# Kernel optimization log

Measured on AMD Instinct MI355X. Metric: run time of the kernel, lower is better.

## Reference

```python
import jax, jax.numpy as jnp
from jax import lax
import numpy as np

BS = 16          # batch (must be even, K % BS == 0)
K = 8192         # MoCo queue size
H = 768          # hidden size
G = 5            # rank_num (number of GMM components)
UPDATE_MEAN = 0.1


def _norm(x):
    return x / jnp.linalg.norm(x, axis=-1, keepdims=True)


def setup_inputs() -> dict:
    key = jax.random.key(0)
    ks = jax.random.split(key, 6)
    sent_q = _norm(jax.random.normal(ks[0], (BS, H), jnp.float32))
    sent_k = _norm(jax.random.normal(ks[1], (BS, H), jnp.float32))
    queue = _norm(jax.random.normal(ks[2], (K, H), jnp.float32))
    mu = jax.random.normal(ks[3], (G, H), jnp.float32)
    lg_sigma2 = jax.random.normal(ks[4], (G, H), jnp.float32)
    pi = jnp.ones((G,), jnp.float32)
    rank_mean = jax.random.uniform(ks[5], (G,), jnp.float32)
    return {"sent_q": sent_q, "sent_k": sent_k, "queue": queue,
            "mu": mu, "lg_sigma2": lg_sigma2, "pi": pi, "rank_mean": rank_mean}


def gaussian_mixture(features, mu, lg_sigma2, pi):
    # features: [B, N, H]; mu/lg_sigma2: [G, H]; pi: [G]
    # expo_{bng} = sum_h (f_{bnh} - mu_{gh})^2 / sigma2_{gh}, expanded so we never
    # materialize the [B, N, G, H] diff tensor the torch code builds.
    inv = jnp.exp(-lg_sigma2)                                   # [G, H]
    expo = (jnp.einsum('bnh,gh->bng', features * features, inv)
            - 2.0 * jnp.einsum('bnh,gh->bng', features, mu * inv)
            + jnp.sum(mu * mu * inv, axis=-1))                  # [B, N, G]
    lg2piD = features.shape[-1] * np.log(2.0 * np.pi).astype(np.float32)
    l_prob = -0.5 * (lg2piD + jnp.sum(lg_sigma2, axis=-1) + expo)
    logits = jax.nn.log_softmax(pi) + l_prob
    logits_norm = logits - jnp.max(logits, axis=-1, keepdims=True)
    prob = jax.nn.softmax(logits_norm, axis=-1)
    return logits_norm, prob


def reference(sent_q, sent_k, queue, mu, lg_sigma2, pi, rank_mean):
    bs = sent_q.shape[0]
    all_feature = jnp.concatenate([sent_k, queue], axis=0)       # [N, H]
    N = all_feature.shape[0]

    # golden mask (is_pair=True): pair j of i is (i + bs//2) mod bs
    pair_label = jnp.concatenate([jnp.arange(bs)[bs // 2:], jnp.arange(bs)[:bs // 2]])
    golden = jnp.arange(bs)[:, None] == pair_label[None, :]      # [bs, bs]
    golden_mask = jnp.concatenate(
        [golden, jnp.zeros((bs, N - bs), bool)], axis=1)         # [bs, N]

    sample_sim = sent_q @ all_feature.T                          # [bs, N]

    # map_scores_to_ranks (rank_mean detached)
    rm = lax.stop_gradient(rank_mean)
    cts_pred = jnp.argmin(jnp.abs(sample_sim[..., None] - rm[None, None, :]), axis=-1)
    cts_dist = jnp.floor((sample_sim + 1.0) / 2.0 * G).astype(jnp.int32)

    # GMM on detached broadcast diff [bs, N, H]
    f = lax.stop_gradient(sent_q)[:, None, :] - lax.stop_gradient(all_feature)[None, :, :]
    gmm_logits, gmm_prob = gaussian_mixture(f, mu, lg_sigma2, pi)
    gmm_pred = jnp.argmax(gmm_prob, axis=-1)                     # [bs, N]

    eye = jnp.arange(bs)[:, None] == jnp.arange(N)[None, :]      # [bs, N]
    # torch: gmm_label aliases cts_pred and is masked_fill_'d in place
    gmm_label = jnp.where(eye | golden_mask, G - 1, cts_pred)

    # update_rank_mean(sample_sim, gmm_pred) -- uses gmm_pred BEFORE cts_label masking
    oh = jax.nn.one_hot(gmm_pred, G, dtype=sample_sim.dtype)     # [bs, N, G]
    counts = jnp.sum(oh, axis=(0, 1))                            # [G]
    sums = jnp.einsum('bng,bn->g', oh, sample_sim)
    cur_rank_mean = sums / (counts + 1e-12)
    upd = (counts != 0).astype(rank_mean.dtype)
    new_rank_mean = (1.0 - upd * UPDATE_MEAN) * rank_mean + upd * UPDATE_MEAN * cur_rank_mean

    # torch: cts_label aliases gmm_pred and masked_fill_ mutates both in place;
    # the returned 'gmm pred' therefore equals this masked version.
    cts_label = jnp.where(golden_mask, G - 1, gmm_pred)

    logits_max = lax.stop_gradient(jnp.max(sample_sim, axis=1, keepdims=True))
    cts_logits = sample_sim - logits_max

    # acc pred: zero the (i, i) entries (torch scatter of 0 at col i)
    acc_pred = sample_sim * (1.0 - eye.astype(sample_sim.dtype))

    return (gmm_logits, gmm_prob, cts_logits, acc_pred, new_rank_mean,
            gmm_label, cts_label, cts_dist)


if __name__ == "__main__":
    outs = reference(**setup_inputs())
    for o in outs:
        print(o.shape, o.dtype)
```

## Files before the change

kernel.cpp:

```cpp
#include <hip/hip_runtime.h>
#include <stdint.h>

#define BS 16
#define KQ 8192
#define NTOT (BS + KQ)
#define H 768
#define G 5
#define UPD 0.1f
#define FPAD 772
#define ROWS 4
#define LG2PID (768.0f * 1.8378770664093453f)

#define SZ_BN   (BS*NTOT)
#define SZ_BNG  (BS*NTOT*G)
#define O_GLOGITS 0
#define O_GPROB   (SZ_BNG)
#define O_CTSLOG  (2*SZ_BNG)
#define O_ACC     (O_CTSLOG + SZ_BN)
#define O_NRM     (O_ACC + SZ_BN)
#define O_GLABEL  (O_NRM + G)
#define O_CLABEL  (O_GLABEL + SZ_BN)
#define O_CDIST   (O_CLABEL + SZ_BN)

#define W_INV   0
#define W_MSC   (G*H)
#define W_BB    (2*G*H)
#define W_CNT8  (W_BB + BS*G)
#define W_SUM8  (W_CNT8 + 128)
#define W_RMX8  (W_SUM8 + 128)
#define W_DIAG  (W_RMX8 + 128)

__device__ __forceinline__ unsigned enc_f(float f) {
    unsigned u = __float_as_uint(f);
    return (u & 0x80000000u) ? ~u : (u | 0x80000000u);
}
__device__ __forceinline__ float dec_f(unsigned k) {
    return (k & 0x80000000u) ? __uint_as_float(k & 0x7fffffffu) : __uint_as_float(~k);
}

__device__ __forceinline__ float wave_red_sum(float v) {
    #pragma unroll
    for (int off = 32; off > 0; off >>= 1) v += __shfl_down(v, off, 64);
    return v;
}

__device__ __forceinline__ void gload_lds16(const float* g, float* l) {
    __builtin_amdgcn_global_load_lds(
        (const __attribute__((address_space(1))) void*)(g),
        (__attribute__((address_space(3))) void*)(l), 16, 0, 0);
}

__global__ __launch_bounds__(256) void prep_kernel(
    const float* __restrict__ sent_q, const float* __restrict__ mu,
    const float* __restrict__ lg,     const float* __restrict__ pi,
    float* __restrict__ ws)
{
    const int t = threadIdx.x;
    const int lane = t & 63;
    const int w = t >> 6;
    const int bx = blockIdx.x;

    if (bx < 20) {
        const int task = bx * 4 + w;
        const int b = task / G, g = task % G;
        float accP = 0.f, accU = 0.f, accC = 0.f, accS = 0.f;
        for (int h = lane; h < H; h += 64) {
            float qv  = sent_q[b*H + h];
            float lgv = lg[g*H + h];
            float m   = mu[g*H + h];
            float iv  = expf(-lgv);
            accP = fmaf(qv*qv, iv, accP);
            accU = fmaf(qv*m,  iv, accU);
            accC = fmaf(m*m,   iv, accC);
            accS += lgv;
        }
        accP = wave_red_sum(accP);
        accU = wave_red_sum(accU);
        accC = wave_red_sum(accC);
        accS = wave_red_sum(accS);
        if (lane == 0) {
            float mx = pi[0];
            #pragma unroll
            for (int gg = 1; gg < G; ++gg) mx = fmaxf(mx, pi[gg]);
            float s = 0.f;
            #pragma unroll
            for (int gg = 0; gg < G; ++gg) s += expf(pi[gg] - mx);
            float lse = mx + logf(s);
            ws[W_BB + task] =
                (pi[g] - lse) - 0.5f*(LG2PID + accS + accC + accP - 2.f*accU);
        }
    } else if (bx < 35) {
        const int i = (bx - 20) * 256 + t;
        float iv = expf(-lg[i]);
        ws[W_INV + i] = iv;
        ws[W_MSC + i] = mu[i] * iv;
    } else {
        for (int i = t; i < 384; i += 256) ws[W_CNT8 + i] = 0.f;
    }
}

__global__ __launch_bounds__(256, 2) void main_kernel(
    const float* __restrict__ sent_q,
    const float* __restrict__ sent_k,
    const float* __restrict__ queue,
    const float* __restrict__ rank_mean,
    const float* __restrict__ invp,
    const float* __restrict__ mscp,
    const float* __restrict__ BBp,
    float* cnt8, float* sum8, unsigned* rmx8, float* diagp,
    float* __restrict__ out)
{
    __shared__ __align__(16) float fbuf[ROWS * FPAD];
    __shared__ float red[64][21];
    __shared__ float s_BB[BS*G];
    __shared__ float s_A2[ROWS*G];
    __shared__ float s_cnt[G], s_sum[G];

    const int t    = threadIdx.x;
    const int lane = t & 63;
    const int w    = t >> 6;
    const int b    = lane >> 2;
    const int nl   = lane & 3;
    const int bx   = blockIdx.x;
    const int n    = bx * ROWS + nl;

    if (t < BS*G) s_BB[t] = BBp[t];
    if (t >= 160 && t < 160 + G) { s_cnt[t-160] = 0.f; s_sum[t-160] = 0.f; }

    {
        const int rn = bx * ROWS + w;
        const float* src = ((rn < BS) ? (sent_k + rn*H) : (queue + (rn - BS)*H)) + lane*4;
        #pragma unroll
        for (int k = 0; k < 3; ++k)
            gload_lds16(src + k*256, &fbuf[w*FPAD + k*256]);
    }
    __syncthreads();

    {
        const float* frow = fbuf + w*FPAD;
        float Tp[G] = {0.f,0.f,0.f,0.f,0.f};
        float Vp[G] = {0.f,0.f,0.f,0.f,0.f};
        #pragma unroll 1
        for (int j = 0; j < 3; ++j) {
            const int h = j*256 + lane*4;
            const float4 fv = *reinterpret_cast<const float4*>(frow + h);
            const float fx2 = fv.x*fv.x, fy2 = fv.y*fv.y, fz2 = fv.z*fv.z, fw2 = fv.w*fv.w;
            #pragma unroll
            for (int g = 0; g < G; ++g) {
                const float4 iv = *reinterpret_cast<const float4*>(invp + g*H + h);
                const float4 mv = *reinterpret_cast<const float4*>(mscp + g*H + h);
                Tp[g] = fmaf(fx2, iv.x, Tp[g]);
                Tp[g] = fmaf(fy2, iv.y, Tp[g]);
                Tp[g] = fmaf(fz2, iv.z, Tp[g]);
                Tp[g] = fmaf(fw2, iv.w, Tp[g]);
                Vp[g] = fmaf(fv.x, mv.x, Vp[g]);
                Vp[g] = fmaf(fv.y, mv.y, Vp[g]);
                Vp[g] = fmaf(fv.z, mv.z, Vp[g]);
                Vp[g] = fmaf(fv.w, mv.w, Vp[g]);
            }
        }
        #pragma unroll
        for (int g = 0; g < G; ++g) {
            float T = wave_red_sum(Tp[g]);
            float V = wave_red_sum(Vp[g]);
            if (lane == 0) s_A2[w*G + g] = 0.5f*T + V;
        }
    }

    const int hu = __builtin_amdgcn_readfirstlane(w * 192);
    const float* qb = sent_q + b*H + hu;
    const float* fb = fbuf + nl*FPAD + hu;
    float sim = 0.f;
    float R[G] = {0.f, 0.f, 0.f, 0.f, 0.f};
    #pragma unroll 4
    for (int i = 0; i < 48; ++i) {
        const float4 qv = *reinterpret_cast<const float4*>(qb + i*4);
        const float4 fv = *reinterpret_cast<const float4*>(fb + i*4);
        float p0 = qv.x * fv.x;
        float p1 = qv.y * fv.y;
        float p2 = qv.z * fv.z;
        float p3 = qv.w * fv.w;
        sim += (p0 + p1) + (p2 + p3);
        #pragma unroll
        for (int g = 0; g < G; ++g) {
            const float* iv = invp + g*H + hu + i*4;
            R[g] = fmaf(p3, iv[3], fmaf(p2, iv[2], fmaf(p1, iv[1], fmaf(p0, iv[0], R[g]))));
        }
    }

    if (w) {
        red[lane][(w-1)*6 + 0] = sim;
        #pragma unroll
        for (int g = 0; g < G; ++g) red[lane][(w-1)*6 + 1 + g] = R[g];
    }
    __syncthreads();

    if (w == 0) {
        #pragma unroll
        for (int qq = 0; qq < 3; ++qq) {
            sim += red[lane][qq*6];
            #pragma unroll
            for (int g = 0; g < G; ++g) R[g] += red[lane][qq*6 + 1 + g];
        }

        float lgt[G];
        #pragma unroll
        for (int g = 0; g < G; ++g)
            lgt[g] = s_BB[b*G + g] - s_A2[nl*G + g] + R[g];
        float mx = lgt[0];
        #pragma unroll
        for (int g = 1; g < G; ++g) mx = fmaxf(mx, lgt[g]);

        const int bn = b * NTOT + n;
        float e[G], se = 0.f;
        #pragma unroll
        for (int g = 0; g < G; ++g) {
            float ln = lgt[g] - mx;
            out[O_GLOGITS + (size_t)bn * G + g] = ln;
            e[g] = expf(ln);
            se += e[g];
        }
        int pred = 0; float bestp = -1.f;
        #pragma unroll
        for (int g = 0; g < G; ++g) {
            float pg = e[g] / se;
            out[O_GPROB + (size_t)bn * G + g] = pg;
            if (pg > bestp) { bestp = pg; pred = g; }
        }

        int cp = 0; float bd = fabsf(sim - rank_mean[0]);
        #pragma unroll
        for (int g = 1; g < G; ++g) {
            float d = fabsf(sim - rank_mean[g]);
            if (d < bd) { bd = d; cp = g; }
        }

        float cdist = floorf((sim + 1.0f) * 0.5f * (float)G);

        bool eyev = (n == b);
        bool gold = (n < BS) && (n == ((b + BS/2) & (BS - 1)));

        out[O_GLABEL + bn] = (eyev || gold) ? (float)(G - 1) : (float)cp;
        out[O_CLABEL + bn] = gold ? (float)(G - 1) : (float)pred;
        out[O_ACC    + bn] = eyev ? 0.f : sim;
        out[O_CDIST  + bn] = cdist;
        if (eyev) diagp[b] = sim;

        atomicAdd(&s_cnt[pred], 1.f);
        atomicAdd(&s_sum[pred], sim);

        float m4 = sim;
        m4 = fmaxf(m4, __shfl_down(m4, 2, 4));
        m4 = fmaxf(m4, __shfl_down(m4, 1, 4));
        if (nl == 0) atomicMax(&rmx8[(bx & 7) * 16 + b], enc_f(m4));
    }
    __syncthreads();
    if (t < G) {
        atomicAdd(&cnt8[(bx & 7) * 16 + t], s_cnt[t]);
        atomicAdd(&sum8[(bx & 7) * 16 + t], s_sum[t]);
    }
}

__global__ __launch_bounds__(256) void final_kernel(
    const float* __restrict__ rank_mean,
    const float* __restrict__ cnt8, const float* __restrict__ sum8,
    const unsigned* __restrict__ rmx8, const float* __restrict__ diagp,
    float* __restrict__ out)
{
    const int i4 = blockIdx.x * 256 + threadIdx.x;
    if (i4 < G) {
        float c = 0.f, s = 0.f;
        #pragma unroll
        for (int j = 0; j < 8; ++j) { c += cnt8[j*16 + i4]; s += sum8[j*16 + i4]; }
        float cur = s / (c + 1e-12f);
        float u = (c != 0.f) ? 1.f : 0.f;
        out[O_NRM + i4] = (1.f - u * UPD) * rank_mean[i4] + u * UPD * cur;
    }
    if (i4 >= SZ_BN/4) return;
    const int i0 = i4 * 4;
    const int b  = i0 / NTOT;
    const int n0 = i0 - b * NTOT;
    unsigned mk = 0u;
    #pragma unroll
    for (int j = 0; j < 8; ++j) mk = max(mk, rmx8[j*16 + b]);
    const float rm = dec_f(mk);
    float4 v = *reinterpret_cast<const float4*>(&out[O_ACC + i0]);
    if (b >= n0 && b < n0 + 4) {
        float d = diagp[b];
        int r = b - n0;
        if (r == 0) v.x = d; else if (r == 1) v.y = d;
        else if (r == 2) v.z = d; else v.w = d;
    }
    float4 o;
    o.x = v.x - rm; o.y = v.y - rm; o.z = v.z - rm; o.w = v.w - rm;
    *reinterpret_cast<float4*>(&out[O_CTSLOG + i0]) = o;
}

extern "C" void kernel_launch(void* const* d_in, const int* in_sizes, int n_in,
                              void* d_out, int out_size, void* d_ws, size_t ws_size,
                              hipStream_t stream) {
    const float* sent_q    = (const float*)d_in[0];
    const float* sent_k    = (const float*)d_in[1];
    const float* queue     = (const float*)d_in[2];
    const float* mu        = (const float*)d_in[3];
    const float* lg        = (const float*)d_in[4];
    const float* pi        = (const float*)d_in[5];
    const float* rank_mean = (const float*)d_in[6];
    float* out = (float*)d_out;
    float* ws  = (float*)d_ws;

    prep_kernel<<<36, 256, 0, stream>>>(sent_q, mu, lg, pi, ws);

    main_kernel<<<NTOT / ROWS, 256, 0, stream>>>(
        sent_q, sent_k, queue, rank_mean,
        ws + W_INV, ws + W_MSC, ws + W_BB,
        ws + W_CNT8, ws + W_SUM8,
        reinterpret_cast<unsigned*>(ws + W_RMX8), ws + W_DIAG,
        out);

    final_kernel<<<(SZ_BN/4 + 255) / 256, 256, 0, stream>>>(
        rank_mean, ws + W_CNT8, ws + W_SUM8,
        reinterpret_cast<const unsigned*>(ws + W_RMX8), ws + W_DIAG,
        out);
}
```

Before: 124.1 us.

## Process eight rows per block with 512 threads and interleaved sent_q layout

Doubles the rows per block to eight, using 512 threads split into two 4-wave halves that share the block's setup and the BB/inverse-sigma loads. A prep step rewrites sent_q into a transposed, batch-interleaved float4 layout in the workspace, so each wave's query loads become contiguous across lanes instead of strided by H. The aim is better coalescing of the query reads and less per-block overhead, at the cost of fewer blocks, more shared memory per block and an extra prep copy.

New measurement: 124.7 us. Within noise of the previous version (+0.4%).

```diff
diff --git a/kernel.cpp b/kernel.cpp
--- a/kernel.cpp
+++ b/kernel.cpp
@@ -8,7 +8,7 @@
 #define G 5
 #define UPD 0.1f
 #define FPAD 772
-#define ROWS 4
+#define ROWS 8
 #define LG2PID (768.0f * 1.8378770664093453f)
 
 #define SZ_BN   (BS*NTOT)
@@ -29,6 +29,7 @@
 #define W_SUM8  (W_CNT8 + 128)
 #define W_RMX8  (W_SUM8 + 128)
 #define W_DIAG  (W_RMX8 + 128)
+#define W_QP    (W_DIAG + BS)
 
 __device__ __forceinline__ unsigned enc_f(float f) {
     unsigned u = __float_as_uint(f);
@@ -94,24 +95,29 @@
         float iv = expf(-lg[i]);
         ws[W_INV + i] = iv;
         ws[W_MSC + i] = mu[i] * iv;
+    } else if (bx == 35) {
+        for (int i = t; i < 384; i += 256) ws[W_CNT8 + i] = 0.f;
     } else {
-        for (int i = t; i < 384; i += 256) ws[W_CNT8 + i] = 0.f;
-    }
-}
-
-__global__ __launch_bounds__(256, 2) void main_kernel(
-    const float* __restrict__ sent_q,
+        const int gid = (bx - 36) * 256 + t;
+        const int i = gid >> 4, b = gid & 15;
+        float4 v = *reinterpret_cast<const float4*>(sent_q + b*H + i*4);
+        reinterpret_cast<float4*>(ws + W_QP)[gid] = v;
+    }
+}
+
+__global__ __launch_bounds__(512, 4) void main_kernel(
     const float* __restrict__ sent_k,
     const float* __restrict__ queue,
     const float* __restrict__ rank_mean,
     const float* __restrict__ invp,
     const float* __restrict__ mscp,
     const float* __restrict__ BBp,
+    const float* __restrict__ qpp,
     float* cnt8, float* sum8, unsigned* rmx8, float* diagp,
     float* __restrict__ out)
 {
     __shared__ __align__(16) float fbuf[ROWS * FPAD];
-    __shared__ float red[64][21];
+    __shared__ float red[2][64][21];
     __shared__ float s_BB[BS*G];
     __shared__ float s_A2[ROWS*G];
     __shared__ float s_cnt[G], s_sum[G];
@@ -119,13 +125,16 @@
     const int t    = threadIdx.x;
     const int lane = t & 63;
     const int w    = t >> 6;
+    const int s    = t >> 8;
+    const int wq   = w & 3;
     const int b    = lane >> 2;
     const int nl   = lane & 3;
+    const int row  = s*4 + nl;
     const int bx   = blockIdx.x;
-    const int n    = bx * ROWS + nl;
+    const int n    = bx * ROWS + row;
 
     if (t < BS*G) s_BB[t] = BBp[t];
-    if (t >= 160 && t < 160 + G) { s_cnt[t-160] = 0.f; s_sum[t-160] = 0.f; }
+    if (t >= 128 && t < 128 + G) { s_cnt[t-128] = 0.f; s_sum[t-128] = 0.f; }
 
     {
         const int rn = bx * ROWS + w;
@@ -167,14 +176,14 @@
         }
     }
 
-    const int hu = __builtin_amdgcn_readfirstlane(w * 192);
-    const float* qb = sent_q + b*H + hu;
-    const float* fb = fbuf + nl*FPAD + hu;
+    const int hu = __builtin_amdgcn_readfirstlane(wq * 192);
+    const float4* q4 = reinterpret_cast<const float4*>(qpp) + (hu >> 2) * 16 + b;
+    const float* fb = fbuf + row*FPAD + hu;
     float sim = 0.f;
     float R[G] = {0.f, 0.f, 0.f, 0.f, 0.f};
     #pragma unroll 4
     for (int i = 0; i < 48; ++i) {
-        const float4 qv = *reinterpret_cast<const float4*>(qb + i*4);
+        const float4 qv = q4[i * 16];
         const float4 fv = *reinterpret_cast<const float4*>(fb + i*4);
         float p0 = qv.x * fv.x;
         float p1 = qv.y * fv.y;
@@ -188,25 +197,25 @@
         }
     }
 
-    if (w) {
-        red[lane][(w-1)*6 + 0] = sim;
-        #pragma unroll
-        for (int g = 0; g < G; ++g) red[lane][(w-1)*6 + 1 + g] = R[g];
+    if (wq) {
+        red[s][lane][(wq-1)*6 + 0] = sim;
+        #pragma unroll
+        for (int g = 0; g < G; ++g) red[s][lane][(wq-1)*6 + 1 + g] = R[g];
     }
     __syncthreads();
 
-    if (w == 0) {
+    if (wq == 0) {
         #pragma unroll
         for (int qq = 0; qq < 3; ++qq) {
-            sim += red[lane][qq*6];
+            sim += red[s][lane][qq*6];
             #pragma unroll
-            for (int g = 0; g < G; ++g) R[g] += red[lane][qq*6 + 1 + g];
+            for (int g = 0; g < G; ++g) R[g] += red[s][lane][qq*6 + 1 + g];
         }
 
         float lgt[G];
         #pragma unroll
         for (int g = 0; g < G; ++g)
-            lgt[g] = s_BB[b*G + g] - s_A2[nl*G + g] + R[g];
+            lgt[g] = s_BB[b*G + g] - s_A2[row*G + g] + R[g];
         float mx = lgt[0];
         #pragma unroll
         for (int g = 1; g < G; ++g) mx = fmaxf(mx, lgt[g]);
@@ -309,11 +318,11 @@
     float* out = (float*)d_out;
     float* ws  = (float*)d_ws;
 
-    prep_kernel<<<36, 256, 0, stream>>>(sent_q, mu, lg, pi, ws);
-
-    main_kernel<<<NTOT / ROWS, 256, 0, stream>>>(
-        sent_q, sent_k, queue, rank_mean,
-        ws + W_INV, ws + W_MSC, ws + W_BB,
+    prep_kernel<<<48, 256, 0, stream>>>(sent_q, mu, lg, pi, ws);
+
+    main_kernel<<<NTOT / ROWS, 512, 0, stream>>>(
+        sent_k, queue, rank_mean,
+        ws + W_INV, ws + W_MSC, ws + W_BB, ws + W_QP,
         ws + W_CNT8, ws + W_SUM8,
         reinterpret_cast<unsigned*>(ws + W_RMX8), ws + W_DIAG,
         out);
```

## Split per-row T/V reduction into separate kernel and drop LDS feature staging

Applied to the files above, without the earlier changes.

Moves the per-feature-row T/V Gaussian reduction into a new tv_kernel that writes A2 to workspace, and the main kernel now reads feature rows directly from global memory instead of staging them in LDS. sent_q is transposed into an interleaved layout in prep_kernel so each lane's query float4 loads are strided by batch. Main kernel launch bounds rise to 4 blocks per SM now that LDS use is lower. The trade-off is an extra kernel launch, each feature row being read twice from global memory, and unstaged global loads in the inner loop.

New measurement: 166.5 us. 1.34x slower.

```diff
diff --git a/kernel.cpp b/kernel.cpp
--- a/kernel.cpp
+++ b/kernel.cpp
@@ -7,8 +7,6 @@
 #define H 768
 #define G 5
 #define UPD 0.1f
-#define FPAD 772
-#define ROWS 4
 #define LG2PID (768.0f * 1.8378770664093453f)
 
 #define SZ_BN   (BS*NTOT)
@@ -29,6 +27,8 @@
 #define W_SUM8  (W_CNT8 + 128)
 #define W_RMX8  (W_SUM8 + 128)
 #define W_DIAG  (W_RMX8 + 128)
+#define W_QP    (W_DIAG + BS)
+#define W_A2    (W_QP + 192*16*4)
 
 __device__ __forceinline__ unsigned enc_f(float f) {
     unsigned u = __float_as_uint(f);
@@ -42,12 +42,6 @@
     #pragma unroll
     for (int off = 32; off > 0; off >>= 1) v += __shfl_down(v, off, 64);
     return v;
-}
-
-__device__ __forceinline__ void gload_lds16(const float* g, float* l) {
-    __builtin_amdgcn_global_load_lds(
-        (const __attribute__((address_space(1))) void*)(g),
-        (__attribute__((address_space(3))) void*)(l), 16, 0, 0);
 }
 
 __global__ __launch_bounds__(256) void prep_kernel(
@@ -94,26 +88,68 @@
         float iv = expf(-lg[i]);
         ws[W_INV + i] = iv;
         ws[W_MSC + i] = mu[i] * iv;
+    } else if (bx == 35) {
+        for (int i = t; i < 384; i += 256) ws[W_CNT8 + i] = 0.f;
     } else {
-        for (int i = t; i < 384; i += 256) ws[W_CNT8 + i] = 0.f;
-    }
-}
-
-__global__ __launch_bounds__(256, 2) void main_kernel(
-    const float* __restrict__ sent_q,
+        const int gid = (bx - 36) * 256 + t;
+        const int i = gid >> 4, b = gid & 15;
+        float4 v = *reinterpret_cast<const float4*>(sent_q + b*H + i*4);
+        reinterpret_cast<float4*>(ws + W_QP)[gid] = v;
+    }
+}
+
+__global__ __launch_bounds__(256) void tv_kernel(
+    const float* __restrict__ sent_k, const float* __restrict__ queue,
+    const float* __restrict__ invp,   const float* __restrict__ mscp,
+    float* __restrict__ A2)
+{
+    const int lane = threadIdx.x & 63;
+    const int n = blockIdx.x * 4 + (threadIdx.x >> 6);
+    const float* f = (n < BS) ? (sent_k + n*H) : (queue + (n - BS) * H);
+
+    float Tp[G] = {0.f,0.f,0.f,0.f,0.f};
+    float Vp[G] = {0.f,0.f,0.f,0.f,0.f};
+    #pragma unroll 1
+    for (int j = 0; j < 3; ++j) {
+        const int h = j*256 + lane*4;
+        const float4 fv = *reinterpret_cast<const float4*>(f + h);
+        const float fx2 = fv.x*fv.x, fy2 = fv.y*fv.y, fz2 = fv.z*fv.z, fw2 = fv.w*fv.w;
+        #pragma unroll
+        for (int g = 0; g < G; ++g) {
+            const float4 iv = *reinterpret_cast<const float4*>(invp + g*H + h);
+            const float4 mv = *reinterpret_cast<const float4*>(mscp + g*H + h);
+            Tp[g] = fmaf(fx2, iv.x, Tp[g]);
+            Tp[g] = fmaf(fy2, iv.y, Tp[g]);
+            Tp[g] = fmaf(fz2, iv.z, Tp[g]);
+            Tp[g] = fmaf(fw2, iv.w, Tp[g]);
+            Vp[g] = fmaf(fv.x, mv.x, Vp[g]);
+            Vp[g] = fmaf(fv.y, mv.y, Vp[g]);
+            Vp[g] = fmaf(fv.z, mv.z, Vp[g]);
+            Vp[g] = fmaf(fv.w, mv.w, Vp[g]);
+        }
+    }
+    #pragma unroll
+    for (int g = 0; g < G; ++g) {
+        float T = wave_red_sum(Tp[g]);
+        float V = wave_red_sum(Vp[g]);
+        if (lane == 0) A2[n*G + g] = 0.5f*T + V;
+    }
+}
+
+__global__ __launch_bounds__(256, 4) void main_kernel(
     const float* __restrict__ sent_k,
     const float* __restrict__ queue,
     const float* __restrict__ rank_mean,
     const float* __restrict__ invp,
-    const float* __restrict__ mscp,
     const float* __restrict__ BBp,
+    const float* __restrict__ A2p,
+    const float* __restrict__ qpp,
     float* cnt8, float* sum8, unsigned* rmx8, float* diagp,
     float* __restrict__ out)
 {
-    __shared__ __align__(16) float fbuf[ROWS * FPAD];
     __shared__ float red[64][21];
     __shared__ float s_BB[BS*G];
-    __shared__ float s_A2[ROWS*G];
+    __shared__ float s_A2[4*G];
     __shared__ float s_cnt[G], s_sum[G];
 
     const int t    = threadIdx.x;
@@ -122,60 +158,22 @@
     const int b    = lane >> 2;
     const int nl   = lane & 3;
     const int bx   = blockIdx.x;
-    const int n    = bx * ROWS + nl;
+    const int n    = bx * 4 + nl;
 
     if (t < BS*G) s_BB[t] = BBp[t];
+    if (t >= 128 && t < 128 + 4*G) s_A2[t-128] = A2p[bx*4*G + (t-128)];
     if (t >= 160 && t < 160 + G) { s_cnt[t-160] = 0.f; s_sum[t-160] = 0.f; }
 
-    {
-        const int rn = bx * ROWS + w;
-        const float* src = ((rn < BS) ? (sent_k + rn*H) : (queue + (rn - BS)*H)) + lane*4;
-        #pragma unroll
-        for (int k = 0; k < 3; ++k)
-            gload_lds16(src + k*256, &fbuf[w*FPAD + k*256]);
-    }
-    __syncthreads();
-
-    {
-        const float* frow = fbuf + w*FPAD;
-        float Tp[G] = {0.f,0.f,0.f,0.f,0.f};
-        float Vp[G] = {0.f,0.f,0.f,0.f,0.f};
-        #pragma unroll 1
-        for (int j = 0; j < 3; ++j) {
-            const int h = j*256 + lane*4;
-            const float4 fv = *reinterpret_cast<const float4*>(frow + h);
-            const float fx2 = fv.x*fv.x, fy2 = fv.y*fv.y, fz2 = fv.z*fv.z, fw2 = fv.w*fv.w;
-            #pragma unroll
-            for (int g = 0; g < G; ++g) {
-                const float4 iv = *reinterpret_cast<const float4*>(invp + g*H + h);
-                const float4 mv = *reinterpret_cast<const float4*>(mscp + g*H + h);
-                Tp[g] = fmaf(fx2, iv.x, Tp[g]);
-                Tp[g] = fmaf(fy2, iv.y, Tp[g]);
-                Tp[g] = fmaf(fz2, iv.z, Tp[g]);
-                Tp[g] = fmaf(fw2, iv.w, Tp[g]);
-                Vp[g] = fmaf(fv.x, mv.x, Vp[g]);
-                Vp[g] = fmaf(fv.y, mv.y, Vp[g]);
-                Vp[g] = fmaf(fv.z, mv.z, Vp[g]);
-                Vp[g] = fmaf(fv.w, mv.w, Vp[g]);
-            }
-        }
-        #pragma unroll
-        for (int g = 0; g < G; ++g) {
-            float T = wave_red_sum(Tp[g]);
-            float V = wave_red_sum(Vp[g]);
-            if (lane == 0) s_A2[w*G + g] = 0.5f*T + V;
-        }
-    }
-
     const int hu = __builtin_amdgcn_readfirstlane(w * 192);
-    const float* qb = sent_q + b*H + hu;
-    const float* fb = fbuf + nl*FPAD + hu;
+    const float* fr = (n < BS) ? (sent_k + n*H) : (queue + (n - BS)*H);
+    const float4* f4 = reinterpret_cast<const float4*>(fr + hu);
+    const float4* q4 = reinterpret_cast<const float4*>(qpp) + (hu >> 2) * 16 + b;
     float sim = 0.f;
     float R[G] = {0.f, 0.f, 0.f, 0.f, 0.f};
     #pragma unroll 4
     for (int i = 0; i < 48; ++i) {
-        const float4 qv = *reinterpret_cast<const float4*>(qb + i*4);
-        const float4 fv = *reinterpret_cast<const float4*>(fb + i*4);
+        const float4 qv = q4[i * 16];
+        const float4 fv = f4[i];
         float p0 = qv.x * fv.x;
         float p1 = qv.y * fv.y;
         float p2 = qv.z * fv.z;
@@ -309,11 +307,14 @@
     float* out = (float*)d_out;
     float* ws  = (float*)d_ws;
 
-    prep_kernel<<<36, 256, 0, stream>>>(sent_q, mu, lg, pi, ws);
-
-    main_kernel<<<NTOT / ROWS, 256, 0, stream>>>(
-        sent_q, sent_k, queue, rank_mean,
-        ws + W_INV, ws + W_MSC, ws + W_BB,
+    prep_kernel<<<48, 256, 0, stream>>>(sent_q, mu, lg, pi, ws);
+
+    tv_kernel<<<NTOT/4, 256, 0, stream>>>(
+        sent_k, queue, ws + W_INV, ws + W_MSC, ws + W_A2);
+
+    main_kernel<<<NTOT/4, 256, 0, stream>>>(
+        sent_k, queue, rank_mean,
+        ws + W_INV, ws + W_BB, ws + W_A2, ws + W_QP,
         ws + W_CNT8, ws + W_SUM8,
         reinterpret_cast<unsigned*>(ws + W_RMX8), ws + W_DIAG,
         out);
```
